# Kernel tuning notes

Measured on AMD Instinct MI355X. Metric: run time of the kernel, lower is better.

Reference implementation:

```python
import jax, jax.numpy as jnp
import numpy as np

B, T, D, HEADS = 2, 2048, 512, 8

def setup_inputs() -> dict:
    key = jax.random.key(0)
    k1, k2 = jax.random.split(key)
    h = jax.random.normal(k1, (B, T, D), dtype=jnp.float32)
    # xavier_uniform over (heads, d, d): fan_in = fan_out = d
    limit = float(np.sqrt(6.0 / (D + D)))
    A = jax.random.uniform(k2, (HEADS, D, D), dtype=jnp.float32, minval=-limit, maxval=limit)
    return {"h": h, "A": A}

def reference(h, A):
    Bb, Tt, d = h.shape
    heads = A.shape[0]
    # per-head bilinear scores: (h @ A_i) @ h^T  -> (B, heads, T, T)
    scores = jnp.einsum('btd,hde,bse->bhts', h, A, h)
    causal = jnp.tril(jnp.ones((Tt, Tt), dtype=bool))  # (T, T)
    scores = jnp.where(causal[None, None], scores, -jnp.inf)
    attn = jax.nn.softmax(scores, axis=-1)  # (B, heads, T, T)
    out = jnp.einsum('bhts,bsd->bhtd', attn, h)  # (B, heads, T, d)
    # torch .view(B, T, -1) on contiguous (B, heads, T, d): raw row-major reshape
    return out.reshape(Bb, Tt, heads * d)
```

## Files before the change

### kernel.cpp

```cpp
#include <hip/hip_runtime.h>

typedef unsigned short ushort_t;
typedef __attribute__((ext_vector_type(8))) short bf16x8;
typedef __attribute__((ext_vector_type(4))) float f32x4;
typedef __attribute__((ext_vector_type(4))) unsigned short u16x4;

#define T_DIM 2048
#define D_DIM 512
#define NH 8
#define NB 2
#define PSTRIDE (2 * T_DIM)

static __device__ __forceinline__ ushort_t f2bf(float x) {
  union { float f; unsigned u; } v; v.f = x;
  unsigned r = v.u + 0x7fffu + ((v.u >> 16) & 1u);
  return (ushort_t)(r >> 16);
}
static __device__ __forceinline__ float bf2f(ushort_t b) {
  union { unsigned u; float f; } v; v.u = ((unsigned)b) << 16;
  return v.f;
}
static __device__ __forceinline__ f32x4 mfma16(bf16x8 a, bf16x8 b, f32x4 c) {
  return __builtin_amdgcn_mfma_f32_16x16x32_bf16(a, b, c, 0, 0, 0);
}

typedef const __attribute__((address_space(1))) unsigned asg_t;
typedef __attribute__((address_space(3))) unsigned asl_t;
static __device__ __forceinline__ void gload16(const ushort_t* g, ushort_t* l) {
  __builtin_amdgcn_global_load_lds((asg_t*)g, (asl_t*)l, 16, 0, 0);
}

static __device__ __forceinline__ void stage128x32(const ushort_t* __restrict__ src,
                                                   size_t ldk, ushort_t* lds, int tid) {
  int w = tid >> 6;
#pragma unroll
  for (int p = 0; p < 2; ++p) {
    int t = p * 256 + tid;
    int r = t >> 2;
    int col = (t & 3) << 3;
    gload16(src + (size_t)r * ldk + col, lds + p * 2048 + (w << 9));
  }
}

__global__ __launch_bounds__(256) void split_h_kernel(const float* __restrict__ h,
    ushort_t* __restrict__ hhi, ushort_t* __restrict__ hlo, ushort_t* __restrict__ hT) {
  __shared__ ushort_t lds[64][68];
  int x = blockIdx.x;
  int b = x >> 8, tt = (x >> 3) & 31, ee = x & 7;
  int t0 = tt * 64, e0 = ee * 64;
  int rr = threadIdx.x >> 4;
  int c4 = (threadIdx.x & 15) * 4;
#pragma unroll
  for (int it = 0; it < 4; ++it) {
    int t = it * 16 + rr;
    size_t idx = ((size_t)(b * T_DIM + t0 + t)) * D_DIM + e0 + c4;
    float4 v = *(const float4*)(h + idx);
    u16x4 hv, lv;
    hv[0] = f2bf(v.x); lv[0] = f2bf(v.x - bf2f(hv[0]));
    hv[1] = f2bf(v.y); lv[1] = f2bf(v.y - bf2f(hv[1]));
    hv[2] = f2bf(v.z); lv[2] = f2bf(v.z - bf2f(hv[2]));
    hv[3] = f2bf(v.w); lv[3] = f2bf(v.w - bf2f(hv[3]));
    *(u16x4*)(hhi + idx) = hv;
    *(u16x4*)(hlo + idx) = lv;
    *(u16x4*)&lds[t][c4] = hv;
  }
  __syncthreads();
#pragma unroll
  for (int it = 0; it < 4; ++it) {
    int e = it * 16 + rr;
    u16x4 wv;
    wv[0] = lds[c4 + 0][e];
    wv[1] = lds[c4 + 1][e];
    wv[2] = lds[c4 + 2][e];
    wv[3] = lds[c4 + 3][e];
    *(u16x4*)(hT + ((size_t)(b * D_DIM + e0 + e)) * T_DIM + t0 + c4) = wv;
  }
}

__global__ __launch_bounds__(256) void split_AT_kernel(const float* __restrict__ A,
    ushort_t* __restrict__ AThi, ushort_t* __restrict__ ATlo) {
  __shared__ ushort_t ldh[64][68];
  __shared__ ushort_t ldl[64][68];
  int x = blockIdx.x;
  int hd = x >> 6, dd = (x >> 3) & 7, ee = x & 7;
  int d0 = dd * 64, e0 = ee * 64;
  int rr = threadIdx.x >> 4;
  int c4 = (threadIdx.x & 15) * 4;
#pragma unroll
  for (int it = 0; it < 4; ++it) {
    int d = it * 16 + rr;
    float4 v = *(const float4*)(A + ((size_t)(hd * D_DIM + d0 + d)) * D_DIM + e0 + c4);
    u16x4 hv, lv;
    hv[0] = f2bf(v.x); lv[0] = f2bf(v.x - bf2f(hv[0]));
    hv[1] = f2bf(v.y); lv[1] = f2bf(v.y - bf2f(hv[1]));
    hv[2] = f2bf(v.z); lv[2] = f2bf(v.z - bf2f(hv[2]));
    hv[3] = f2bf(v.w); lv[3] = f2bf(v.w - bf2f(hv[3]));
    *(u16x4*)&ldh[d][c4] = hv;
    *(u16x4*)&ldl[d][c4] = lv;
  }
  __syncthreads();
#pragma unroll
  for (int it = 0; it < 4; ++it) {
    int e = it * 16 + rr;
    u16x4 wh, wl;
    wh[0] = ldh[c4 + 0][e]; wl[0] = ldl[c4 + 0][e];
    wh[1] = ldh[c4 + 1][e]; wl[1] = ldl[c4 + 1][e];
    wh[2] = ldh[c4 + 2][e]; wl[2] = ldl[c4 + 2][e];
    wh[3] = ldh[c4 + 3][e]; wl[3] = ldl[c4 + 3][e];
    size_t o = ((size_t)(hd * D_DIM + e0 + e)) * D_DIM + d0 + c4;
    *(u16x4*)(AThi + o) = wh;
    *(u16x4*)(ATlo + o) = wl;
  }
}

__global__ __launch_bounds__(256, 2) void qgemm_kernel(
    const ushort_t* __restrict__ hhi, const ushort_t* __restrict__ hlo,
    const ushort_t* __restrict__ AThi, const ushort_t* __restrict__ ATlo,
    ushort_t* __restrict__ Qhi, ushort_t* __restrict__ Qlo) {
  __shared__ ushort_t lAh[128 * 32], lAl[128 * 32], lBh[128 * 32], lBl[128 * 32];
  int bid = blockIdx.x;
  int hd = bid & 7;
  int rem = bid >> 3;
  int nt = rem & 3;
  int mt = (rem >> 2) & 15;
  int b = rem >> 6;
  int bh = b * NH + hd;
  int tid = threadIdx.x;
  int w = tid >> 6, lane = tid & 63;
  int g = lane >> 4, c = lane & 15;
  int m0 = (w >> 1) * 64, n0 = (w & 1) * 64;
  const ushort_t* Ah = hhi + (size_t)b * T_DIM * D_DIM + (size_t)(mt * 128) * D_DIM;
  const ushort_t* Al = hlo + (size_t)b * T_DIM * D_DIM + (size_t)(mt * 128) * D_DIM;
  const ushort_t* Bh = AThi + (size_t)hd * D_DIM * D_DIM + (size_t)(nt * 128) * D_DIM;
  const ushort_t* Bl = ATlo + (size_t)hd * D_DIM * D_DIM + (size_t)(nt * 128) * D_DIM;
  f32x4 zero4 = {0.f, 0.f, 0.f, 0.f};
  f32x4 acc[4][4];
#pragma unroll
  for (int i = 0; i < 4; ++i)
#pragma unroll
    for (int j = 0; j < 4; ++j) acc[i][j] = zero4;
  for (int kc = 0; kc < 16; ++kc) {
    int k0 = kc * 32;
    stage128x32(Ah + k0, D_DIM, lAh, tid);
    stage128x32(Al + k0, D_DIM, lAl, tid);
    stage128x32(Bh + k0, D_DIM, lBh, tid);
    stage128x32(Bl + k0, D_DIM, lBl, tid);
    __syncthreads();
    bf16x8 ah[4], al[4], bh8[4], bl8[4];
#pragma unroll
    for (int mf = 0; mf < 4; ++mf) {
      int ro = (m0 + 16 * mf + c) * 32 + g * 8;
      ah[mf] = *(const bf16x8*)&lAh[ro];
      al[mf] = *(const bf16x8*)&lAl[ro];
    }
#pragma unroll
    for (int nf = 0; nf < 4; ++nf) {
      int ro = (n0 + 16 * nf + c) * 32 + g * 8;
      bh8[nf] = *(const bf16x8*)&lBh[ro];
      bl8[nf] = *(const bf16x8*)&lBl[ro];
    }
#pragma unroll
    for (int mf = 0; mf < 4; ++mf)
#pragma unroll
      for (int nf = 0; nf < 4; ++nf) {
        acc[mf][nf] = mfma16(ah[mf], bh8[nf], acc[mf][nf]);
        acc[mf][nf] = mfma16(ah[mf], bl8[nf], acc[mf][nf]);
        acc[mf][nf] = mfma16(al[mf], bh8[nf], acc[mf][nf]);
      }
    __syncthreads();
  }
  size_t qbase = (size_t)bh * T_DIM * D_DIM;
#pragma unroll
  for (int mf = 0; mf < 4; ++mf)
#pragma unroll
    for (int nf = 0; nf < 4; ++nf)
#pragma unroll
      for (int i2 = 0; i2 < 4; ++i2) {
        int q = mt * 128 + m0 + 16 * mf + 4 * g + i2;
        int e = nt * 128 + n0 + 16 * nf + c;
        float v = acc[mf][nf][i2];
        ushort_t hi = f2bf(v);
        ushort_t lo = f2bf(v - bf2f(hi));
        Qhi[qbase + (size_t)q * D_DIM + e] = hi;
        Qlo[qbase + (size_t)q * D_DIM + e] = lo;
      }
}

__global__ __launch_bounds__(256, 2) void sgemm_kernel(
    const ushort_t* __restrict__ Qhi, const ushort_t* __restrict__ Qlo,
    const ushort_t* __restrict__ Khi, const ushort_t* __restrict__ Klo,
    float* __restrict__ S, int b, int hd0) {
  __shared__ ushort_t lAh[128 * 32], lAl[128 * 32], lBh[128 * 32], lBl[128 * 32];
  int nhc = gridDim.x / 136;
  int i = blockIdx.x;
  int hdl = i % nhc, ti = i / nhc;
  int tq = (int)((sqrtf(8.f * (float)ti + 1.f) - 1.f) * 0.5f);
  while ((tq + 1) * (tq + 2) / 2 <= ti) ++tq;
  while (tq * (tq + 1) / 2 > ti) --tq;
  int ts = ti - tq * (tq + 1) / 2;
  int bh = b * NH + hd0 + hdl;
  int tid = threadIdx.x;
  int w = tid >> 6, lane = tid & 63;
  int g = lane >> 4, c = lane & 15;
  int m0 = (w >> 1) * 64, n0 = (w & 1) * 64;
  const ushort_t* Ah = Qhi + (size_t)bh * T_DIM * D_DIM + (size_t)(tq * 128) * D_DIM;
  const ushort_t* Al = Qlo + (size_t)bh * T_DIM * D_DIM + (size_t)(tq * 128) * D_DIM;
  const ushort_t* Bh = Khi + (size_t)b * T_DIM * D_DIM + (size_t)(ts * 128) * D_DIM;
  const ushort_t* Bl = Klo + (size_t)b * T_DIM * D_DIM + (size_t)(ts * 128) * D_DIM;
  f32x4 zero4 = {0.f, 0.f, 0.f, 0.f};
  f32x4 acc[4][4];
#pragma unroll
  for (int ii = 0; ii < 4; ++ii)
#pragma unroll
    for (int j = 0; j < 4; ++j) acc[ii][j] = zero4;
  for (int kc = 0; kc < 16; ++kc) {
    int k0 = kc * 32;
    stage128x32(Ah + k0, D_DIM, lAh, tid);
    stage128x32(Al + k0, D_DIM, lAl, tid);
    stage128x32(Bh + k0, D_DIM, lBh, tid);
    stage128x32(Bl + k0, D_DIM, lBl, tid);
    __syncthreads();
    bf16x8 ah[4], al[4], bh8[4], bl8[4];
#pragma unroll
    for (int mf = 0; mf < 4; ++mf) {
      int ro = (m0 + 16 * mf + c) * 32 + g * 8;
      ah[mf] = *(const bf16x8*)&lAh[ro];
      al[mf] = *(const bf16x8*)&lAl[ro];
    }
#pragma unroll
    for (int nf = 0; nf < 4; ++nf) {
      int ro = (n0 + 16 * nf + c) * 32 + g * 8;
      bh8[nf] = *(const bf16x8*)&lBh[ro];
      bl8[nf] = *(const bf16x8*)&lBl[ro];
    }
#pragma unroll
    for (int mf = 0; mf < 4; ++mf)
#pragma unroll
      for (int nf = 0; nf < 4; ++nf) {
        acc[mf][nf] = mfma16(ah[mf], bh8[nf], acc[mf][nf]);
        acc[mf][nf] = mfma16(ah[mf], bl8[nf], acc[mf][nf]);
        acc[mf][nf] = mfma16(al[mf], bh8[nf], acc[mf][nf]);
      }
    __syncthreads();
  }
#pragma unroll
  for (int mf = 0; mf < 4; ++mf)
#pragma unroll
    for (int nf = 0; nf < 4; ++nf)
#pragma unroll
      for (int i2 = 0; i2 < 4; ++i2) {
        int q = tq * 128 + m0 + 16 * mf + 4 * g + i2;
        int s = ts * 128 + n0 + 16 * nf + c;
        S[((size_t)(hdl * T_DIM + q)) * T_DIM + s] = acc[mf][nf][i2];
      }
}

__global__ __launch_bounds__(256) void softmax_kernel(float* __restrict__ S) {
  __shared__ float rowbuf[2048];
  __shared__ float red[4];
  int nhc = gridDim.x >> 11;
  int i = blockIdx.x;
  int hdl = i % nhc, q = i / nhc;
  float* srow = S + ((size_t)(hdl * T_DIM + q)) * T_DIM;
  ushort_t* prow = (ushort_t*)srow;
  int n = q + 1;
  int nout = ((q >> 7) + 1) << 7;
  int tid = threadIdx.x;
  float mx = -3.0e38f;
  for (int s0 = tid * 4; s0 < nout; s0 += 1024) {
    float4 v = make_float4(-3.0e38f, -3.0e38f, -3.0e38f, -3.0e38f);
    if (s0 < n) v = *(const float4*)(srow + s0);
    float a0 = (s0 + 0 < n) ? v.x : -3.0e38f;
    float a1 = (s0 + 1 < n) ? v.y : -3.0e38f;
    float a2 = (s0 + 2 < n) ? v.z : -3.0e38f;
    float a3 = (s0 + 3 < n) ? v.w : -3.0e38f;
    rowbuf[s0 + 0] = a0; rowbuf[s0 + 1] = a1;
    rowbuf[s0 + 2] = a2; rowbuf[s0 + 3] = a3;
    mx = fmaxf(mx, fmaxf(fmaxf(a0, a1), fmaxf(a2, a3)));
  }
#pragma unroll
  for (int off = 1; off < 64; off <<= 1) mx = fmaxf(mx, __shfl_xor(mx, off));
  if ((tid & 63) == 0) red[tid >> 6] = mx;
  __syncthreads();
  mx = fmaxf(fmaxf(red[0], red[1]), fmaxf(red[2], red[3]));
  float sum = 0.f;
  for (int s0 = tid * 4; s0 < nout; s0 += 1024) {
    float e0 = __expf(rowbuf[s0 + 0] - mx);
    float e1 = __expf(rowbuf[s0 + 1] - mx);
    float e2 = __expf(rowbuf[s0 + 2] - mx);
    float e3 = __expf(rowbuf[s0 + 3] - mx);
    rowbuf[s0 + 0] = e0; rowbuf[s0 + 1] = e1;
    rowbuf[s0 + 2] = e2; rowbuf[s0 + 3] = e3;
    sum += (e0 + e1) + (e2 + e3);
  }
#pragma unroll
  for (int off = 1; off < 64; off <<= 1) sum += __shfl_xor(sum, off);
  __syncthreads();
  if ((tid & 63) == 0) red[tid >> 6] = sum;
  __syncthreads();
  float inv = 1.0f / ((red[0] + red[1]) + (red[2] + red[3]));
  for (int s0 = tid * 4; s0 < nout; s0 += 1024) {
    u16x4 o;
    o[0] = f2bf(rowbuf[s0 + 0] * inv);
    o[1] = f2bf(rowbuf[s0 + 1] * inv);
    o[2] = f2bf(rowbuf[s0 + 2] * inv);
    o[3] = f2bf(rowbuf[s0 + 3] * inv);
    *(u16x4*)(prow + s0) = o;
  }
}

__global__ __launch_bounds__(256, 2) void pv_kernel(const ushort_t* __restrict__ P,
    const ushort_t* __restrict__ hT, float* __restrict__ out, int b, int hd0, int nhc) {
  __shared__ ushort_t lA[128 * 32], lB[128 * 32];
  int i = blockIdx.x;
  int hdl = i % nhc;
  int rem = i / nhc;
  int nt = rem & 3;
  int tq = 15 - (rem >> 2);
  int tid = threadIdx.x;
  int w = tid >> 6, lane = tid & 63;
  int g = lane >> 4, c = lane & 15;
  int m0 = (w >> 1) * 64, n0 = (w & 1) * 64;
  const ushort_t* Ab = P + (size_t)(hdl * T_DIM + tq * 128) * PSTRIDE;
  const ushort_t* Bb = hT + (size_t)b * D_DIM * T_DIM + (size_t)(nt * 128) * T_DIM;
  f32x4 zero4 = {0.f, 0.f, 0.f, 0.f};
  f32x4 acc[4][4];
#pragma unroll
  for (int ii = 0; ii < 4; ++ii)
#pragma unroll
    for (int j = 0; j < 4; ++j) acc[ii][j] = zero4;
  int nk = (tq + 1) * 4;
  for (int kc = 0; kc < nk; ++kc) {
    int k0 = kc * 32;
    stage128x32(Ab + k0, PSTRIDE, lA, tid);
    stage128x32(Bb + k0, T_DIM, lB, tid);
    __syncthreads();
    bf16x8 af[4], bf[4];
#pragma unroll
    for (int mf = 0; mf < 4; ++mf) af[mf] = *(const bf16x8*)&lA[(m0 + 16 * mf + c) * 32 + g * 8];
#pragma unroll
    for (int nf = 0; nf < 4; ++nf) bf[nf] = *(const bf16x8*)&lB[(n0 + 16 * nf + c) * 32 + g * 8];
#pragma unroll
    for (int mf = 0; mf < 4; ++mf)
#pragma unroll
      for (int nf = 0; nf < 4; ++nf) acc[mf][nf] = mfma16(af[mf], bf[nf], acc[mf][nf]);
    __syncthreads();
  }
  size_t obase = (size_t)(b * NH + hd0 + hdl) * T_DIM * D_DIM;
#pragma unroll
  for (int mf = 0; mf < 4; ++mf)
#pragma unroll
    for (int nf = 0; nf < 4; ++nf)
#pragma unroll
      for (int i2 = 0; i2 < 4; ++i2) {
        int q = tq * 128 + m0 + 16 * mf + 4 * g + i2;
        int d = nt * 128 + n0 + 16 * nf + c;
        out[obase + (size_t)q * D_DIM + d] = acc[mf][nf][i2];
      }
}

extern "C" void kernel_launch(void* const* d_in, const int* in_sizes, int n_in,
                              void* d_out, int out_size, void* d_ws, size_t ws_size,
                              hipStream_t stream) {
  const float* h = (const float*)d_in[0];
  const float* A = (const float*)d_in[1];
  float* out = (float*)d_out;
  char* ws = (char*)d_ws;
  const size_t SZ_H = (size_t)NB * T_DIM * D_DIM * sizeof(ushort_t);
  const size_t SZ_A = (size_t)NH * D_DIM * D_DIM * sizeof(ushort_t);
  const size_t SZ_Q = (size_t)NB * NH * T_DIM * D_DIM * sizeof(ushort_t);
  const size_t SZ_S1 = (size_t)T_DIM * T_DIM * sizeof(float);
  const size_t FIXED = 3 * SZ_H + 2 * SZ_A + 2 * SZ_Q;
  ushort_t* hhi  = (ushort_t*)(ws);
  ushort_t* hlo  = (ushort_t*)(ws + SZ_H);
  ushort_t* hT   = (ushort_t*)(ws + 2 * SZ_H);
  ushort_t* AThi = (ushort_t*)(ws + 3 * SZ_H);
  ushort_t* ATlo = (ushort_t*)(ws + 3 * SZ_H + SZ_A);
  ushort_t* Qhi  = (ushort_t*)(ws + 3 * SZ_H + 2 * SZ_A);
  ushort_t* Qlo  = (ushort_t*)(ws + 3 * SZ_H + 2 * SZ_A + SZ_Q);
  float*    Sbuf = (float*)   (ws + FIXED);

  int nhc = NH;
  while (nhc > 1 && FIXED + (size_t)nhc * SZ_S1 > ws_size) nhc >>= 1;

  split_h_kernel<<<512, 256, 0, stream>>>(h, hhi, hlo, hT);
  split_AT_kernel<<<512, 256, 0, stream>>>(A, AThi, ATlo);
  qgemm_kernel<<<1024, 256, 0, stream>>>(hhi, hlo, AThi, ATlo, Qhi, Qlo);
  for (int b = 0; b < NB; ++b) {
    for (int hc = 0; hc < NH; hc += nhc) {
      sgemm_kernel<<<nhc * 136, 256, 0, stream>>>(Qhi, Qlo, hhi, hlo, Sbuf, b, hc);
      softmax_kernel<<<nhc * T_DIM, 256, 0, stream>>>(Sbuf);
      pv_kernel<<<nhc * 64, 256, 0, stream>>>((const ushort_t*)Sbuf, hT, out, b, hc, nhc);
    }
  }
}
```

Measured before the change: 399.4 us.

## Double-buffer LDS tiles in qgemm, sgemm and pv GEMM kernels

Allocates two LDS buffers per operand in the three GEMM kernels and prefetches the next K-chunk with global_load_lds while the current chunk is read and fed to MFMA. This removes the barrier that sat between staging and compute, so global-load latency can overlap with matrix math. It doubles LDS use per block (64 KB in the split-precision kernels), which may limit occupancy. Correctness also relies on the remaining end-of-iteration barrier waiting for the outstanding async loads.

```diff
diff --git a/kernel.cpp b/kernel.cpp
--- a/kernel.cpp
+++ b/kernel.cpp
@@ -10,6 +10,7 @@
 #define NH 8
 #define NB 2
 #define PSTRIDE (2 * T_DIM)
+#define TILE_E 4096
 
 static __device__ __forceinline__ ushort_t f2bf(float x) {
   union { float f; unsigned u; } v; v.f = x;
@@ -117,7 +118,7 @@
     const ushort_t* __restrict__ hhi, const ushort_t* __restrict__ hlo,
     const ushort_t* __restrict__ AThi, const ushort_t* __restrict__ ATlo,
     ushort_t* __restrict__ Qhi, ushort_t* __restrict__ Qlo) {
-  __shared__ ushort_t lAh[128 * 32], lAl[128 * 32], lBh[128 * 32], lBl[128 * 32];
+  __shared__ ushort_t lAh[2 * TILE_E], lAl[2 * TILE_E], lBh[2 * TILE_E], lBl[2 * TILE_E];
   int bid = blockIdx.x;
   int hd = bid & 7;
   int rem = bid >> 3;
@@ -139,23 +140,31 @@
   for (int i = 0; i < 4; ++i)
 #pragma unroll
     for (int j = 0; j < 4; ++j) acc[i][j] = zero4;
+  stage128x32(Ah, D_DIM, lAh, tid);
+  stage128x32(Al, D_DIM, lAl, tid);
+  stage128x32(Bh, D_DIM, lBh, tid);
+  stage128x32(Bl, D_DIM, lBl, tid);
+  __syncthreads();
   for (int kc = 0; kc < 16; ++kc) {
-    int k0 = kc * 32;
-    stage128x32(Ah + k0, D_DIM, lAh, tid);
-    stage128x32(Al + k0, D_DIM, lAl, tid);
-    stage128x32(Bh + k0, D_DIM, lBh, tid);
-    stage128x32(Bl + k0, D_DIM, lBl, tid);
-    __syncthreads();
+    int cur = (kc & 1) ? TILE_E : 0;
+    int nxt = cur ^ TILE_E;
+    if (kc < 15) {
+      int k0 = (kc + 1) * 32;
+      stage128x32(Ah + k0, D_DIM, lAh + nxt, tid);
+      stage128x32(Al + k0, D_DIM, lAl + nxt, tid);
+      stage128x32(Bh + k0, D_DIM, lBh + nxt, tid);
+      stage128x32(Bl + k0, D_DIM, lBl + nxt, tid);
+    }
     bf16x8 ah[4], al[4], bh8[4], bl8[4];
 #pragma unroll
     for (int mf = 0; mf < 4; ++mf) {
-      int ro = (m0 + 16 * mf + c) * 32 + g * 8;
+      int ro = cur + (m0 + 16 * mf + c) * 32 + g * 8;
       ah[mf] = *(const bf16x8*)&lAh[ro];
       al[mf] = *(const bf16x8*)&lAl[ro];
     }
 #pragma unroll
     for (int nf = 0; nf < 4; ++nf) {
-      int ro = (n0 + 16 * nf + c) * 32 + g * 8;
+      int ro = cur + (n0 + 16 * nf + c) * 32 + g * 8;
       bh8[nf] = *(const bf16x8*)&lBh[ro];
       bl8[nf] = *(const bf16x8*)&lBl[ro];
     }
@@ -190,7 +199,7 @@
     const ushort_t* __restrict__ Qhi, const ushort_t* __restrict__ Qlo,
     const ushort_t* __restrict__ Khi, const ushort_t* __restrict__ Klo,
     float* __restrict__ S, int b, int hd0) {
-  __shared__ ushort_t lAh[128 * 32], lAl[128 * 32], lBh[128 * 32], lBl[128 * 32];
+  __shared__ ushort_t lAh[2 * TILE_E], lAl[2 * TILE_E], lBh[2 * TILE_E], lBl[2 * TILE_E];
   int nhc = gridDim.x / 136;
   int i = blockIdx.x;
   int hdl = i % nhc, ti = i / nhc;
@@ -213,23 +222,31 @@
   for (int ii = 0; ii < 4; ++ii)
 #pragma unroll
     for (int j = 0; j < 4; ++j) acc[ii][j] = zero4;
+  stage128x32(Ah, D_DIM, lAh, tid);
+  stage128x32(Al, D_DIM, lAl, tid);
+  stage128x32(Bh, D_DIM, lBh, tid);
+  stage128x32(Bl, D_DIM, lBl, tid);
+  __syncthreads();
   for (int kc = 0; kc < 16; ++kc) {
-    int k0 = kc * 32;
-    stage128x32(Ah + k0, D_DIM, lAh, tid);
-    stage128x32(Al + k0, D_DIM, lAl, tid);
-    stage128x32(Bh + k0, D_DIM, lBh, tid);
-    stage128x32(Bl + k0, D_DIM, lBl, tid);
-    __syncthreads();
+    int cur = (kc & 1) ? TILE_E : 0;
+    int nxt = cur ^ TILE_E;
+    if (kc < 15) {
+      int k0 = (kc + 1) * 32;
+      stage128x32(Ah + k0, D_DIM, lAh + nxt, tid);
+      stage128x32(Al + k0, D_DIM, lAl + nxt, tid);
+      stage128x32(Bh + k0, D_DIM, lBh + nxt, tid);
+      stage128x32(Bl + k0, D_DIM, lBl + nxt, tid);
+    }
     bf16x8 ah[4], al[4], bh8[4], bl8[4];
 #pragma unroll
     for (int mf = 0; mf < 4; ++mf) {
-      int ro = (m0 + 16 * mf + c) * 32 + g * 8;
+      int ro = cur + (m0 + 16 * mf + c) * 32 + g * 8;
       ah[mf] = *(const bf16x8*)&lAh[ro];
       al[mf] = *(const bf16x8*)&lAl[ro];
     }
 #pragma unroll
     for (int nf = 0; nf < 4; ++nf) {
-      int ro = (n0 + 16 * nf + c) * 32 + g * 8;
+      int ro = cur + (n0 + 16 * nf + c) * 32 + g * 8;
       bh8[nf] = *(const bf16x8*)&lBh[ro];
       bl8[nf] = *(const bf16x8*)&lBl[ro];
     }
@@ -311,7 +328,7 @@
 
 __global__ __launch_bounds__(256, 2) void pv_kernel(const ushort_t* __restrict__ P,
     const ushort_t* __restrict__ hT, float* __restrict__ out, int b, int hd0, int nhc) {
-  __shared__ ushort_t lA[128 * 32], lB[128 * 32];
+  __shared__ ushort_t lA[2 * TILE_E], lB[2 * TILE_E];
   int i = blockIdx.x;
   int hdl = i % nhc;
   int rem = i / nhc;
@@ -330,16 +347,24 @@
 #pragma unroll
     for (int j = 0; j < 4; ++j) acc[ii][j] = zero4;
   int nk = (tq + 1) * 4;
+  stage128x32(Ab, PSTRIDE, lA, tid);
+  stage128x32(Bb, T_DIM, lB, tid);
+  __syncthreads();
   for (int kc = 0; kc < nk; ++kc) {
-    int k0 = kc * 32;
-    stage128x32(Ab + k0, PSTRIDE, lA, tid);
-    stage128x32(Bb + k0, T_DIM, lB, tid);
-    __syncthreads();
+    int cur = (kc & 1) ? TILE_E : 0;
+    int nxt = cur ^ TILE_E;
+    if (kc + 1 < nk) {
+      int k0 = (kc + 1) * 32;
+      stage128x32(Ab + k0, PSTRIDE, lA + nxt, tid);
+      stage128x32(Bb + k0, T_DIM, lB + nxt, tid);
+    }
     bf16x8 af[4], bf[4];
 #pragma unroll
-    for (int mf = 0; mf < 4; ++mf) af[mf] = *(const bf16x8*)&lA[(m0 + 16 * mf + c) * 32 + g * 8];
-#pragma unroll
-    for (int nf = 0; nf < 4; ++nf) bf[nf] = *(const bf16x8*)&lB[(n0 + 16 * nf + c) * 32 + g * 8];
+    for (int mf = 0; mf < 4; ++mf)
+      af[mf] = *(const bf16x8*)&lA[cur + (m0 + 16 * mf + c) * 32 + g * 8];
+#pragma unroll
+    for (int nf = 0; nf < 4; ++nf)
+      bf[nf] = *(const bf16x8*)&lB[cur + (n0 + 16 * nf + c) * 32 + g * 8];
 #pragma unroll
     for (int mf = 0; mf < 4; ++mf)
 #pragma unroll
```

New measurement: 406.2 us. About the same (+1.7%).

## Store causal scores in packed 128x128 tile slots and batch both batches per launch

Applied to the files above, without the earlier changes.

Score storage changes from full dense T×T rows per head to packed lower-triangular 128×128 tile slots (136 per head). This drops the unused upper-triangle memory and makes sgemm writes contiguous per tile. The smaller footprint lets both batches and all heads run in a single sgemm/softmax/pv launch sequence instead of per-batch or per-head-chunk loops, which cuts launch count and gives larger grids. Softmax and pv now compute per-tile addresses, so rows are no longer contiguous across tiles and the address math gets more complex.

```diff
diff --git a/kernel.cpp b/kernel.cpp
--- a/kernel.cpp
+++ b/kernel.cpp
@@ -9,7 +9,8 @@
 #define D_DIM 512
 #define NH 8
 #define NB 2
-#define PSTRIDE (2 * T_DIM)
+#define SLOT_F 16384
+#define SLOT_U 32768
 
 static __device__ __forceinline__ ushort_t f2bf(float x) {
   union { float f; unsigned u; } v; v.f = x;
@@ -40,6 +41,10 @@
     int col = (t & 3) << 3;
     gload16(src + (size_t)r * ldk + col, lds + p * 2048 + (w << 9));
   }
+}
+
+static __device__ __forceinline__ void decode_bh(int j, int nbc, int& bl, int& hd) {
+  if (nbc == 2) { bl = j & 1; hd = j >> 1; } else { bl = 0; hd = j; }
 }
 
 __global__ __launch_bounds__(256) void split_h_kernel(const float* __restrict__ h,
@@ -189,16 +194,20 @@
 __global__ __launch_bounds__(256, 2) void sgemm_kernel(
     const ushort_t* __restrict__ Qhi, const ushort_t* __restrict__ Qlo,
     const ushort_t* __restrict__ Khi, const ushort_t* __restrict__ Klo,
-    float* __restrict__ S, int b, int hd0) {
+    float* __restrict__ S, int b0, int nbc) {
   __shared__ ushort_t lAh[128 * 32], lAl[128 * 32], lBh[128 * 32], lBl[128 * 32];
-  int nhc = gridDim.x / 136;
+  int mlanes = nbc * 8;
   int i = blockIdx.x;
-  int hdl = i % nhc, ti = i / nhc;
+  int j = i % mlanes, ti = i / mlanes;
+  int bl, hd;
+  decode_bh(j, nbc, bl, hd);
+  int b = b0 + bl;
+  int bh = b * NH + hd;
+  int bhl = bl * NH + hd;
   int tq = (int)((sqrtf(8.f * (float)ti + 1.f) - 1.f) * 0.5f);
   while ((tq + 1) * (tq + 2) / 2 <= ti) ++tq;
   while (tq * (tq + 1) / 2 > ti) --tq;
   int ts = ti - tq * (tq + 1) / 2;
-  int bh = b * NH + hd0 + hdl;
   int tid = threadIdx.x;
   int w = tid >> 6, lane = tid & 63;
   int g = lane >> 4, c = lane & 15;
@@ -212,7 +221,7 @@
 #pragma unroll
   for (int ii = 0; ii < 4; ++ii)
 #pragma unroll
-    for (int j = 0; j < 4; ++j) acc[ii][j] = zero4;
+    for (int jj = 0; jj < 4; ++jj) acc[ii][jj] = zero4;
   for (int kc = 0; kc < 16; ++kc) {
     int k0 = kc * 32;
     stage128x32(Ah + k0, D_DIM, lAh, tid);
@@ -243,33 +252,40 @@
       }
     __syncthreads();
   }
+  float* Sslot = S + ((size_t)(bhl * 136 + tq * (tq + 1) / 2 + ts)) * SLOT_F;
 #pragma unroll
   for (int mf = 0; mf < 4; ++mf)
 #pragma unroll
     for (int nf = 0; nf < 4; ++nf)
 #pragma unroll
       for (int i2 = 0; i2 < 4; ++i2) {
-        int q = tq * 128 + m0 + 16 * mf + 4 * g + i2;
-        int s = ts * 128 + n0 + 16 * nf + c;
-        S[((size_t)(hdl * T_DIM + q)) * T_DIM + s] = acc[mf][nf][i2];
+        int lq = m0 + 16 * mf + 4 * g + i2;
+        int ls = n0 + 16 * nf + c;
+        Sslot[(size_t)lq * 128 + ls] = acc[mf][nf][i2];
       }
 }
 
-__global__ __launch_bounds__(256) void softmax_kernel(float* __restrict__ S) {
+__global__ __launch_bounds__(256) void softmax_kernel(float* __restrict__ S, int nbc) {
   __shared__ float rowbuf[2048];
   __shared__ float red[4];
-  int nhc = gridDim.x >> 11;
+  int mlanes = nbc * 8;
   int i = blockIdx.x;
-  int hdl = i % nhc, q = i / nhc;
-  float* srow = S + ((size_t)(hdl * T_DIM + q)) * T_DIM;
-  ushort_t* prow = (ushort_t*)srow;
+  int j = i % mlanes, q = i / mlanes;
+  int bl, hd;
+  decode_bh(j, nbc, bl, hd);
+  int bhl = bl * NH + hd;
+  int tq = q >> 7, lq = q & 127;
+  float* Sb = S + (size_t)bhl * 136 * SLOT_F;
+  size_t rowf = (size_t)(tq * (tq + 1) / 2) * SLOT_F + (size_t)lq * 128;
   int n = q + 1;
-  int nout = ((q >> 7) + 1) << 7;
+  int nout = (tq + 1) << 7;
   int tid = threadIdx.x;
   float mx = -3.0e38f;
   for (int s0 = tid * 4; s0 < nout; s0 += 1024) {
+    int ts = s0 >> 7;
+    const float* src = Sb + rowf + (size_t)ts * SLOT_F + (s0 & 127);
     float4 v = make_float4(-3.0e38f, -3.0e38f, -3.0e38f, -3.0e38f);
-    if (s0 < n) v = *(const float4*)(srow + s0);
+    if (s0 < n) v = *(const float4*)src;
     float a0 = (s0 + 0 < n) ? v.x : -3.0e38f;
     float a1 = (s0 + 1 < n) ? v.y : -3.0e38f;
     float a2 = (s0 + 2 < n) ? v.z : -3.0e38f;
@@ -300,53 +316,62 @@
   __syncthreads();
   float inv = 1.0f / ((red[0] + red[1]) + (red[2] + red[3]));
   for (int s0 = tid * 4; s0 < nout; s0 += 1024) {
+    int ts = s0 >> 7;
+    ushort_t* dst = (ushort_t*)Sb + 2 * (rowf + (size_t)ts * SLOT_F) + (s0 & 127);
     u16x4 o;
     o[0] = f2bf(rowbuf[s0 + 0] * inv);
     o[1] = f2bf(rowbuf[s0 + 1] * inv);
     o[2] = f2bf(rowbuf[s0 + 2] * inv);
     o[3] = f2bf(rowbuf[s0 + 3] * inv);
-    *(u16x4*)(prow + s0) = o;
+    *(u16x4*)dst = o;
   }
 }
 
 __global__ __launch_bounds__(256, 2) void pv_kernel(const ushort_t* __restrict__ P,
-    const ushort_t* __restrict__ hT, float* __restrict__ out, int b, int hd0, int nhc) {
+    const ushort_t* __restrict__ hT, float* __restrict__ out, int b0, int nbc) {
   __shared__ ushort_t lA[128 * 32], lB[128 * 32];
+  int mlanes = nbc * 8;
   int i = blockIdx.x;
-  int hdl = i % nhc;
-  int rem = i / nhc;
+  int j = i % mlanes;
+  int rem = i / mlanes;
   int nt = rem & 3;
   int tq = 15 - (rem >> 2);
+  int bl, hd;
+  decode_bh(j, nbc, bl, hd);
+  int b = b0 + bl;
+  int bhl = bl * NH + hd;
   int tid = threadIdx.x;
   int w = tid >> 6, lane = tid & 63;
   int g = lane >> 4, c = lane & 15;
   int m0 = (w >> 1) * 64, n0 = (w & 1) * 64;
-  const ushort_t* Ab = P + (size_t)(hdl * T_DIM + tq * 128) * PSTRIDE;
+  size_t pslot = (size_t)(bhl * 136 + tq * (tq + 1) / 2);
   const ushort_t* Bb = hT + (size_t)b * D_DIM * T_DIM + (size_t)(nt * 128) * T_DIM;
   f32x4 zero4 = {0.f, 0.f, 0.f, 0.f};
   f32x4 acc[4][4];
 #pragma unroll
   for (int ii = 0; ii < 4; ++ii)
 #pragma unroll
-    for (int j = 0; j < 4; ++j) acc[ii][j] = zero4;
+    for (int jj = 0; jj < 4; ++jj) acc[ii][jj] = zero4;
   int nk = (tq + 1) * 4;
   for (int kc = 0; kc < nk; ++kc) {
-    int k0 = kc * 32;
-    stage128x32(Ab + k0, PSTRIDE, lA, tid);
-    stage128x32(Bb + k0, T_DIM, lB, tid);
+    const ushort_t* Asrc = P + (pslot + (kc >> 2)) * SLOT_U + ((kc & 3) << 5);
+    stage128x32(Asrc, 256, lA, tid);
+    stage128x32(Bb + kc * 32, T_DIM, lB, tid);
     __syncthreads();
     bf16x8 af[4], bf[4];
 #pragma unroll
-    for (int mf = 0; mf < 4; ++mf) af[mf] = *(const bf16x8*)&lA[(m0 + 16 * mf + c) * 32 + g * 8];
-#pragma unroll
-    for (int nf = 0; nf < 4; ++nf) bf[nf] = *(const bf16x8*)&lB[(n0 + 16 * nf + c) * 32 + g * 8];
-#pragma unroll
     for (int mf = 0; mf < 4; ++mf)
+      af[mf] = *(const bf16x8*)&lA[(m0 + 16 * mf + c) * 32 + g * 8];
+#pragma unroll
+    for (int nf = 0; nf < 4; ++nf)
+      bf[nf] = *(const bf16x8*)&lB[(n0 + 16 * nf + c) * 32 + g * 8];
+#pragma unroll
+    for (int mf = 0; mf < 4; ++mf)
 #pragma unroll
       for (int nf = 0; nf < 4; ++nf) acc[mf][nf] = mfma16(af[mf], bf[nf], acc[mf][nf]);
     __syncthreads();
   }
-  size_t obase = (size_t)(b * NH + hd0 + hdl) * T_DIM * D_DIM;
+  size_t obase = (size_t)((b * NH + hd)) * T_DIM * D_DIM;
 #pragma unroll
   for (int mf = 0; mf < 4; ++mf)
 #pragma unroll
@@ -369,7 +394,7 @@
   const size_t SZ_H = (size_t)NB * T_DIM * D_DIM * sizeof(ushort_t);
   const size_t SZ_A = (size_t)NH * D_DIM * D_DIM * sizeof(ushort_t);
   const size_t SZ_Q = (size_t)NB * NH * T_DIM * D_DIM * sizeof(ushort_t);
-  const size_t SZ_S1 = (size_t)T_DIM * T_DIM * sizeof(float);
+  const size_t SZ_SB = 136ull * SLOT_F * sizeof(float) * NH;
   const size_t FIXED = 3 * SZ_H + 2 * SZ_A + 2 * SZ_Q;
   ushort_t* hhi  = (ushort_t*)(ws);
   ushort_t* hlo  = (ushort_t*)(ws + SZ_H);
@@ -380,17 +405,14 @@
   ushort_t* Qlo  = (ushort_t*)(ws + 3 * SZ_H + 2 * SZ_A + SZ_Q);
   float*    Sbuf = (float*)   (ws + FIXED);
 
-  int nhc = NH;
-  while (nhc > 1 && FIXED + (size_t)nhc * SZ_S1 > ws_size) nhc >>= 1;
+  int nbc = (FIXED + 2 * SZ_SB <= ws_size) ? 2 : 1;
 
   split_h_kernel<<<512, 256, 0, stream>>>(h, hhi, hlo, hT);
   split_AT_kernel<<<512, 256, 0, stream>>>(A, AThi, ATlo);
   qgemm_kernel<<<1024, 256, 0, stream>>>(hhi, hlo, AThi, ATlo, Qhi, Qlo);
-  for (int b = 0; b < NB; ++b) {
-    for (int hc = 0; hc < NH; hc += nhc) {
-      sgemm_kernel<<<nhc * 136, 256, 0, stream>>>(Qhi, Qlo, hhi, hlo, Sbuf, b, hc);
-      softmax_kernel<<<nhc * T_DIM, 256, 0, stream>>>(Sbuf);
-      pv_kernel<<<nhc * 64, 256, 0, stream>>>((const ushort_t*)Sbuf, hT, out, b, hc, nhc);
-    }
-  }
-}
+  for (int b0 = 0; b0 < NB; b0 += nbc) {
+    sgemm_kernel<<<nbc * 8 * 136, 256, 0, stream>>>(Qhi, Qlo, hhi, hlo, Sbuf, b0, nbc);
+    softmax_kernel<<<nbc * 8 * 2048, 256, 0, stream>>>(Sbuf, nbc);
+    pv_kernel<<<nbc * 512, 256, 0, stream>>>((const ushort_t*)Sbuf, hT, out, b0, nbc);
+  }
+}
```

After: 354.3 us. 11.3% less time.
